# Kernel optimization log

Hardware: AMD Instinct MI355X
Metric: run time of the kernel (lower is better)

Reference implementation:

```python
import jax, jax.numpy as jnp
import numpy as np
from jax import lax

F8 = jnp.float8_e4m3fn


def setup_inputs() -> dict:
    key = jax.random.key(0)
    kx, kw = jax.random.split(key)
    x = jax.random.normal(kx, (2, 128, 4, 192, 320), dtype=jnp.float32)
    # matches reset_parameters: normal(0, 0.02) then cast to fp8
    weight = jax.random.normal(kw, (128, 128, 3, 3, 3), dtype=jnp.float32) * 0.02
    return {"x": x, "weight": weight}


def reference(x, weight):
    # fp8 e4m3 quantization round-trip (the torch module stores/consumes fp8),
    # compute/accumulate in fp32 as an fp8 conv kernel would.
    xq = x.astype(F8).astype(jnp.float32)
    wq = weight.astype(F8).astype(jnp.float32)
    # causal temporal padding: (kT-1, 0) = (2, 0); spatial 'same' padding (1,1)
    xp = jnp.pad(xq, ((0, 0), (0, 0), (2, 0), (1, 1), (1, 1)))
    out = lax.conv_general_dilated(
        xp, wq,
        window_strides=(1, 1, 1),
        padding='VALID',
        dimension_numbers=('NCDHW', 'OIDHW', 'NCDHW'),
    )  # (B, 128, 4, 192, 320)
    return out
```

## Files before the change

kernel.cpp:

```cpp
#include <hip/hip_runtime.h>
#include <hip/hip_fp8.h>


using f32x16 = __attribute__((ext_vector_type(16))) float;
using i32x8 = __attribute__((ext_vector_type(8))) int;
using i32x4 = __attribute__((ext_vector_type(4))) int;
typedef long long i64;
struct alignas(16) L2v { i64 x, y; };

namespace {
constexpr int Cc = 128, Dd = 4, Hh = 192, Ww = 320;
constexpr int HP = 194, WP = 322;
constexpr int NTAP = 27;
constexpr size_t PLANE = (size_t)4 * WP * 32;
constexpr size_t XQ_BYTES = (size_t)2 * Dd * HP * PLANE;
constexpr int ZA = 8 * 2 * 2576;
constexpr int ZB = 8 * 192 * 32;
constexpr int GSTR = WP * 32;
constexpr int HB = 1056;
constexpr int KDSTR = 9 * 2 * 4 * 64 * 32;
constexpr int NQX = 5 * 192 * 8;
constexpr int NZP = (ZA + ZB + 255) / 256;
constexpr int NWP = (Cc * Cc * NTAP + 255) / 256;
}

__global__ __launch_bounds__(256) void prep_kernel(const float* __restrict__ x,
                                                   const float* __restrict__ w,
                                                   unsigned char* __restrict__ xq,
                                                   unsigned char* __restrict__ wpk) {
  const int id = blockIdx.x;
  const int tid = threadIdx.x;
  if (id < NQX) {
    __shared__ unsigned char lt[64 * 136];
    const int wx = id % 5;
    const int h = (id / 5) % 192;
    const int bd = id / 960;
    const int b = bd >> 2, d = bd & 3;
    const int w0 = wx * 64;
    const int wl = tid & 63, cig = tid >> 6;
    const size_t cstr = (size_t)Dd * Hh * Ww;
    const float* xp = x + (((size_t)b * Cc * Dd + d) * Hh + h) * Ww + w0 + wl;
    #pragma unroll 4
    for (int i = 0; i < 32; ++i) {
      int ci = cig * 32 + i;
      __hip_fp8_e4m3 q(xp[ci * cstr]);
      lt[wl * 136 + ci] = q.__x;
    }
    __syncthreads();
    unsigned char* plane = xq + ((size_t)(b * Dd + d) * HP + h + 1) * PLANE;
    int g = tid >> 6, ww = tid & 63;
    const unsigned char* src = lt + ww * 136 + g * 32;
    i64 a0 = *(const i64*)(src), a1 = *(const i64*)(src + 8);
    i64 a2 = *(const i64*)(src + 16), a3 = *(const i64*)(src + 24);
    unsigned char* dst = plane + (size_t)g * GSTR + (size_t)(w0 + 1 + ww) * 32;
    *(L2v*)dst = L2v{a0, a1};
    *(L2v*)(dst + 16) = L2v{a2, a3};
  } else if (id < NQX + NZP) {
    int i = (id - NQX) * 256 + tid;
    if (i < ZA) {
      int bd = i / (2 * 2576);
      int r = i - bd * (2 * 2576);
      int hsel = r / 2576, seg = r - hsel * 2576;
      L2v z{0, 0};
      *(L2v*)(xq + ((size_t)bd * HP + (hsel ? 193 : 0)) * PLANE + (size_t)seg * 16) = z;
    } else if (i < ZA + ZB) {
      int j = i - ZA;
      int bd = j / (192 * 32);
      int r = j - bd * (192 * 32);
      int h = r / 32 + 1;
      int t = r & 31;
      int g = t >> 3, s2 = t & 7;
      int wsel = s2 >> 2, part = s2 & 3;
      *(i64*)(xq + ((size_t)bd * HP + h) * PLANE + (size_t)g * GSTR
              + (size_t)(wsel ? 321 : 0) * 32 + part * 8) = 0;
    }
  } else {
    int idx = (id - NQX - NZP) * 256 + tid;
    if (idx < Cc * Cc * NTAP) {
      int tap = idx % NTAP;
      int t = idx / NTAP;
      int ci = t % Cc, co = t / Cc;
      int cc = ci >> 6, cq = co >> 5;
      int lane = (((ci >> 5) & 1) << 5) | (co & 31);
      __hip_fp8_e4m3 q(w[idx]);
      wpk[((((size_t)tap * 2 + cc) * 4 + cq) * 64 + lane) * 32 + (ci & 31)] = q.__x;
    }
  }
}

__global__ __launch_bounds__(256, 2) void conv_mfma(const unsigned char* __restrict__ xq,
                                                    const unsigned char* __restrict__ wpk,
                                                    float* __restrict__ out) {
  __shared__ unsigned char lb[4 * 4 * 2 * HB];
  const int tid = threadIdx.x;
  const int lane = tid & 63, wv = tid >> 6;
  const int l31 = lane & 31, chalf = lane >> 5;
  const int hr = wv >> 1, ch = wv & 1;
  const int id = blockIdx.x;
  const int xcd = id & 7, j = id >> 3;
  const int h0l = j / 40, rem = j - h0l * 40;
  const int z = rem / 5, wx = rem - z * 5;
  const int b = z >> 2, dout = z & 3;
  const int h0 = (xcd * 12 + h0l) * 2;
  const int w0 = wx * 64;
  const int kdmin = dout >= 2 ? 0 : 2 - dout;

  const long imgstep = (long)HP * PLANE;
  const long img0 = (long)(b * Dd + dout - 2) * imgstep;
  const unsigned char* vbase = wpk + ch * 4096 + lane * 32;

  const unsigned char* bb[3];
  #pragma unroll
  for (int kw = 0; kw < 3; ++kw)
    bb[kw] = lb + (hr * 4 + chalf) * 2 * HB + (l31 + kw) * 16;

  f32x16 acc[2][2];
  #pragma unroll
  for (int a = 0; a < 2; ++a)
    #pragma unroll
    for (int n = 0; n < 2; ++n)
      #pragma unroll
      for (int r = 0; r < 16; ++r) acc[a][n][r] = 0.f;

  i32x8 av[3][2];

  for (int kd = kdmin; kd < 3; ++kd) {
    __syncthreads();
    const unsigned char* img = xq + img0 + (long)kd * imgstep;
    for (int u = tid; u < 1056; u += 256) {
      int w = u % 66, rest = u / 66;
      int g = rest & 3, hrow = rest >> 2;
      const unsigned char* src = img + (size_t)(h0 + hrow) * PLANE
          + (size_t)g * GSTR + (size_t)(w0 + w) * 32;
      L2v lo = *(const L2v*)src;
      L2v hi = *(const L2v*)(src + 16);
      unsigned char* base = lb + (hrow * 4 + g) * 2 * HB + w * 16;
      *(L2v*)(base) = lo;
      *(L2v*)(base + HB) = hi;
    }
    const unsigned char* wkd = vbase + (size_t)kd * KDSTR;
    #pragma unroll
    for (int t = 0; t < 2; ++t) {
      const int kh = t / 6, cc = (t / 3) % 2, kw = t % 3;
      #pragma unroll
      for (int ct = 0; ct < 2; ++ct)
        av[t][ct] = *(const i32x8*)(wkd + (kh * 3 + kw) * 16384 + cc * 8192 + ct * 2048);
    }
    asm volatile("s_waitcnt lgkmcnt(0)" ::: "memory");
    __builtin_amdgcn_s_barrier();
    __builtin_amdgcn_sched_barrier(0);

    __builtin_amdgcn_s_setprio(1);
    #pragma unroll
    for (int t = 0; t < 18; ++t) {
      const int kh = t / 6, cc = (t / 3) % 2, kw = t % 3;
      if (t < 16) {
        const int tp = t + 2;
        const int khp = tp / 6, ccp = (tp / 3) % 2, kwp = tp % 3;
        #pragma unroll
        for (int ct = 0; ct < 2; ++ct)
          av[tp % 3][ct] =
              *(const i32x8*)(wkd + (khp * 3 + kwp) * 16384 + ccp * 8192 + ct * 2048);
      }
      i32x8 bv[2];
      #pragma unroll
      for (int nf = 0; nf < 2; ++nf) {
        const int off = (kh * 4 + cc * 2) * 2 * HB + nf * 512;
        i32x4 blo = *(const i32x4*)(bb[kw] + off);
        i32x4 bhi = *(const i32x4*)(bb[kw] + off + HB);
        bv[nf] = __builtin_shufflevector(blo, bhi, 0, 1, 2, 3, 4, 5, 6, 7);
      }
      if (t < 16)      asm volatile("s_waitcnt vmcnt(4)" ::: "memory");
      else if (t == 16) asm volatile("s_waitcnt vmcnt(2)" ::: "memory");
      else              asm volatile("s_waitcnt vmcnt(0)" ::: "memory");
      asm volatile("s_waitcnt lgkmcnt(0)" ::: "memory");
      __builtin_amdgcn_sched_barrier(0);
      #pragma unroll
      for (int nf = 0; nf < 2; ++nf)
        #pragma unroll
        for (int ct = 0; ct < 2; ++ct)
          acc[ct][nf] = __builtin_amdgcn_mfma_scale_f32_32x32x64_f8f6f4(
              av[t % 3][ct], bv[nf], acc[ct][nf], 0, 0, 0, 127, 0, 127);
    }
    __builtin_amdgcn_s_setprio(0);
  }

  #pragma unroll
  for (int ct = 0; ct < 2; ++ct)
    #pragma unroll
    for (int nf = 0; nf < 2; ++nf) {
      int ww = w0 + nf * 32 + l31;
      #pragma unroll
      for (int reg = 0; reg < 16; ++reg) {
        int co = ch * 64 + ct * 32 + (reg & 3) + 8 * (reg >> 2) + 4 * chalf;
        out[(((size_t)b * Cc + co) * Dd + dout) * (size_t)(Hh * Ww)
            + (size_t)(h0 + hr) * Ww + ww] = acc[ct][nf][reg];
      }
    }
}

extern "C" void kernel_launch(void* const* d_in, const int* in_sizes, int n_in,
                              void* d_out, int out_size, void* d_ws, size_t ws_size,
                              hipStream_t stream) {
  const float* x = (const float*)d_in[0];
  const float* w = (const float*)d_in[1];
  unsigned char* xq = (unsigned char*)d_ws;
  unsigned char* wpk = xq + XQ_BYTES;
  float* out = (float*)d_out;

  prep_kernel<<<dim3(NQX + NZP + NWP), 256, 0, stream>>>(x, w, xq, wpk);
  conv_mfma<<<dim3(3840), 256, 0, stream>>>(xq, wpk, out);
}
```

Before: 222.9 us.

## Double-buffer LDS and weight fragments, drop manual waitcnts, raise occupancy to 3

```diff
diff --git a/kernel.cpp b/kernel.cpp
--- a/kernel.cpp
+++ b/kernel.cpp
@@ -88,7 +88,7 @@
   }
 }
 
-__global__ __launch_bounds__(256, 2) void conv_mfma(const unsigned char* __restrict__ xq,
+__global__ __launch_bounds__(256, 3) void conv_mfma(const unsigned char* __restrict__ xq,
                                                     const unsigned char* __restrict__ wpk,
                                                     float* __restrict__ out) {
   __shared__ unsigned char lb[4 * 4 * 2 * HB];
@@ -122,7 +122,28 @@
       #pragma unroll
       for (int r = 0; r < 16; ++r) acc[a][n][r] = 0.f;
 
-  i32x8 av[3][2];
+  i32x8 bvd[2][2];
+  i32x8 avd[2][2];
+
+#define LOADB(PAR, T)                                                          \
+  {                                                                            \
+    constexpr int kh_ = (T) / 6, cc_ = ((T) / 3) % 2, kw_ = (T) % 3;           \
+    _Pragma("unroll")                                                          \
+    for (int nf = 0; nf < 2; ++nf) {                                           \
+      const int off_ = (kh_ * 4 + cc_ * 2) * 2 * HB + nf * 512;                \
+      i32x4 blo_ = *(const i32x4*)(bb[kw_] + off_);                            \
+      i32x4 bhi_ = *(const i32x4*)(bb[kw_] + off_ + HB);                       \
+      bvd[PAR][nf] = __builtin_shufflevector(blo_, bhi_, 0, 1, 2, 3, 4, 5, 6, 7); \
+    }                                                                          \
+  }
+#define LOADA(PAR, T)                                                          \
+  {                                                                            \
+    constexpr int kh_ = (T) / 6, cc_ = ((T) / 3) % 2, kw_ = (T) % 3;           \
+    _Pragma("unroll")                                                          \
+    for (int ct = 0; ct < 2; ++ct)                                             \
+      avd[PAR][ct] = *(const i32x8*)(wkd + (kh_ * 3 + kw_) * 16384             \
+                                     + cc_ * 8192 + ct * 2048);                \
+  }
 
   for (int kd = kdmin; kd < 3; ++kd) {
     __syncthreads();
@@ -138,52 +159,46 @@
       *(L2v*)(base) = lo;
       *(L2v*)(base + HB) = hi;
     }
+    __syncthreads();
+
     const unsigned char* wkd = vbase + (size_t)kd * KDSTR;
-    #pragma unroll
-    for (int t = 0; t < 2; ++t) {
-      const int kh = t / 6, cc = (t / 3) % 2, kw = t % 3;
-      #pragma unroll
-      for (int ct = 0; ct < 2; ++ct)
-        av[t][ct] = *(const i32x8*)(wkd + (kh * 3 + kw) * 16384 + cc * 8192 + ct * 2048);
-    }
-    asm volatile("s_waitcnt lgkmcnt(0)" ::: "memory");
-    __builtin_amdgcn_s_barrier();
-    __builtin_amdgcn_sched_barrier(0);
-
+    LOADB(0, 0)
+    LOADA(0, 0)
     __builtin_amdgcn_s_setprio(1);
     #pragma unroll
     for (int t = 0; t < 18; ++t) {
-      const int kh = t / 6, cc = (t / 3) % 2, kw = t % 3;
-      if (t < 16) {
-        const int tp = t + 2;
-        const int khp = tp / 6, ccp = (tp / 3) % 2, kwp = tp % 3;
-        #pragma unroll
-        for (int ct = 0; ct < 2; ++ct)
-          av[tp % 3][ct] =
-              *(const i32x8*)(wkd + (khp * 3 + kwp) * 16384 + ccp * 8192 + ct * 2048);
+      const int p = t & 1, q = p ^ 1;
+      switch (t) {
+        case 0:  LOADB(1, 1)  LOADA(1, 1)  break;
+        case 1:  LOADB(0, 2)  LOADA(0, 2)  break;
+        case 2:  LOADB(1, 3)  LOADA(1, 3)  break;
+        case 3:  LOADB(0, 4)  LOADA(0, 4)  break;
+        case 4:  LOADB(1, 5)  LOADA(1, 5)  break;
+        case 5:  LOADB(0, 6)  LOADA(0, 6)  break;
+        case 6:  LOADB(1, 7)  LOADA(1, 7)  break;
+        case 7:  LOADB(0, 8)  LOADA(0, 8)  break;
+        case 8:  LOADB(1, 9)  LOADA(1, 9)  break;
+        case 9:  LOADB(0, 10) LOADA(0, 10) break;
+        case 10: LOADB(1, 11) LOADA(1, 11) break;
+        case 11: LOADB(0, 12) LOADA(0, 12) break;
+        case 12: LOADB(1, 13) LOADA(1, 13) break;
+        case 13: LOADB(0, 14) LOADA(0, 14) break;
+        case 14: LOADB(1, 15) LOADA(1, 15) break;
+        case 15: LOADB(0, 16) LOADA(0, 16) break;
+        case 16: LOADB(1, 17) LOADA(1, 17) break;
+        default: break;
       }
-      i32x8 bv[2];
-      #pragma unroll
-      for (int nf = 0; nf < 2; ++nf) {
-        const int off = (kh * 4 + cc * 2) * 2 * HB + nf * 512;
-        i32x4 blo = *(const i32x4*)(bb[kw] + off);
-        i32x4 bhi = *(const i32x4*)(bb[kw] + off + HB);
-        bv[nf] = __builtin_shufflevector(blo, bhi, 0, 1, 2, 3, 4, 5, 6, 7);
-      }
-      if (t < 16)      asm volatile("s_waitcnt vmcnt(4)" ::: "memory");
-      else if (t == 16) asm volatile("s_waitcnt vmcnt(2)" ::: "memory");
-      else              asm volatile("s_waitcnt vmcnt(0)" ::: "memory");
-      asm volatile("s_waitcnt lgkmcnt(0)" ::: "memory");
-      __builtin_amdgcn_sched_barrier(0);
       #pragma unroll
       for (int nf = 0; nf < 2; ++nf)
         #pragma unroll
         for (int ct = 0; ct < 2; ++ct)
           acc[ct][nf] = __builtin_amdgcn_mfma_scale_f32_32x32x64_f8f6f4(
-              av[t % 3][ct], bv[nf], acc[ct][nf], 0, 0, 0, 127, 0, 127);
+              avd[p][ct], bvd[p][nf], acc[ct][nf], 0, 0, 0, 127, 0, 127);
     }
     __builtin_amdgcn_s_setprio(0);
   }
+#undef LOADB
+#undef LOADA
 
   #pragma unroll
   for (int ct = 0; ct < 2; ++ct)
```

Result: no change. 225.7 us (+1.3%).

## Give each wave all 128 output channels over four output rows per block

Applied to the files above, without the earlier changes.

```diff
diff --git a/kernel.cpp b/kernel.cpp
--- a/kernel.cpp
+++ b/kernel.cpp
@@ -91,108 +91,91 @@
 __global__ __launch_bounds__(256, 2) void conv_mfma(const unsigned char* __restrict__ xq,
                                                     const unsigned char* __restrict__ wpk,
                                                     float* __restrict__ out) {
-  __shared__ unsigned char lb[4 * 4 * 2 * HB];
+  __shared__ unsigned char lb[6 * 4 * 2 * HB];
   const int tid = threadIdx.x;
-  const int lane = tid & 63, wv = tid >> 6;
+  const int lane = tid & 63;
+  const int hr = tid >> 6;
   const int l31 = lane & 31, chalf = lane >> 5;
-  const int hr = wv >> 1, ch = wv & 1;
   const int id = blockIdx.x;
   const int xcd = id & 7, j = id >> 3;
   const int h0l = j / 40, rem = j - h0l * 40;
   const int z = rem / 5, wx = rem - z * 5;
   const int b = z >> 2, dout = z & 3;
-  const int h0 = (xcd * 12 + h0l) * 2;
+  const int h0 = (xcd * 6 + h0l) * 4;
   const int w0 = wx * 64;
   const int kdmin = dout >= 2 ? 0 : 2 - dout;
 
   const long imgstep = (long)HP * PLANE;
   const long img0 = (long)(b * Dd + dout - 2) * imgstep;
-  const unsigned char* vbase = wpk + ch * 4096 + lane * 32;
+  const unsigned char* vbase = wpk + lane * 32;
 
   const unsigned char* bb[3];
   #pragma unroll
   for (int kw = 0; kw < 3; ++kw)
-    bb[kw] = lb + (hr * 4 + chalf) * 2 * HB + (l31 + kw) * 16;
+    bb[kw] = lb + hr * 8448 + chalf * 2112 + (l31 + kw) * 16;
 
-  f32x16 acc[2][2];
+  f32x16 acc[4][2];
   #pragma unroll
-  for (int a = 0; a < 2; ++a)
+  for (int a = 0; a < 4; ++a)
     #pragma unroll
     for (int n = 0; n < 2; ++n)
       #pragma unroll
       for (int r = 0; r < 16; ++r) acc[a][n][r] = 0.f;
 
-  i32x8 av[3][2];
-
   for (int kd = kdmin; kd < 3; ++kd) {
     __syncthreads();
     const unsigned char* img = xq + img0 + (long)kd * imgstep;
-    for (int u = tid; u < 1056; u += 256) {
+    for (int u = tid; u < 1584; u += 256) {
       int w = u % 66, rest = u / 66;
       int g = rest & 3, hrow = rest >> 2;
       const unsigned char* src = img + (size_t)(h0 + hrow) * PLANE
           + (size_t)g * GSTR + (size_t)(w0 + w) * 32;
       L2v lo = *(const L2v*)src;
       L2v hi = *(const L2v*)(src + 16);
-      unsigned char* base = lb + (hrow * 4 + g) * 2 * HB + w * 16;
+      unsigned char* base = lb + rest * 2112 + w * 16;
       *(L2v*)(base) = lo;
       *(L2v*)(base + HB) = hi;
     }
+    __syncthreads();
+
     const unsigned char* wkd = vbase + (size_t)kd * KDSTR;
-    #pragma unroll
-    for (int t = 0; t < 2; ++t) {
-      const int kh = t / 6, cc = (t / 3) % 2, kw = t % 3;
-      #pragma unroll
-      for (int ct = 0; ct < 2; ++ct)
-        av[t][ct] = *(const i32x8*)(wkd + (kh * 3 + kw) * 16384 + cc * 8192 + ct * 2048);
-    }
-    asm volatile("s_waitcnt lgkmcnt(0)" ::: "memory");
-    __builtin_amdgcn_s_barrier();
-    __builtin_amdgcn_sched_barrier(0);
-
     __builtin_amdgcn_s_setprio(1);
     #pragma unroll
-    for (int t = 0; t < 18; ++t) {
-      const int kh = t / 6, cc = (t / 3) % 2, kw = t % 3;
-      if (t < 16) {
-        const int tp = t + 2;
-        const int khp = tp / 6, ccp = (tp / 3) % 2, kwp = tp % 3;
+    for (int kh = 0; kh < 3; ++kh)
+      #pragma unroll
+      for (int cc = 0; cc < 2; ++cc)
         #pragma unroll
-        for (int ct = 0; ct < 2; ++ct)
-          av[tp % 3][ct] =
-              *(const i32x8*)(wkd + (khp * 3 + kwp) * 16384 + ccp * 8192 + ct * 2048);
-      }
-      i32x8 bv[2];
-      #pragma unroll
-      for (int nf = 0; nf < 2; ++nf) {
-        const int off = (kh * 4 + cc * 2) * 2 * HB + nf * 512;
-        i32x4 blo = *(const i32x4*)(bb[kw] + off);
-        i32x4 bhi = *(const i32x4*)(bb[kw] + off + HB);
-        bv[nf] = __builtin_shufflevector(blo, bhi, 0, 1, 2, 3, 4, 5, 6, 7);
-      }
-      if (t < 16)      asm volatile("s_waitcnt vmcnt(4)" ::: "memory");
-      else if (t == 16) asm volatile("s_waitcnt vmcnt(2)" ::: "memory");
-      else              asm volatile("s_waitcnt vmcnt(0)" ::: "memory");
-      asm volatile("s_waitcnt lgkmcnt(0)" ::: "memory");
-      __builtin_amdgcn_sched_barrier(0);
-      #pragma unroll
-      for (int nf = 0; nf < 2; ++nf)
-        #pragma unroll
-        for (int ct = 0; ct < 2; ++ct)
-          acc[ct][nf] = __builtin_amdgcn_mfma_scale_f32_32x32x64_f8f6f4(
-              av[t % 3][ct], bv[nf], acc[ct][nf], 0, 0, 0, 127, 0, 127);
-    }
+        for (int kw = 0; kw < 3; ++kw) {
+          i32x8 av[4];
+          #pragma unroll
+          for (int ct = 0; ct < 4; ++ct)
+            av[ct] = *(const i32x8*)(wkd + (kh * 3 + kw) * 16384 + cc * 8192 + ct * 2048);
+          i32x8 bv[2];
+          #pragma unroll
+          for (int nf = 0; nf < 2; ++nf) {
+            const int off = kh * 8448 + cc * 4224 + nf * 512;
+            i32x4 blo = *(const i32x4*)(bb[kw] + off);
+            i32x4 bhi = *(const i32x4*)(bb[kw] + off + HB);
+            bv[nf] = __builtin_shufflevector(blo, bhi, 0, 1, 2, 3, 4, 5, 6, 7);
+          }
+          #pragma unroll
+          for (int nf = 0; nf < 2; ++nf)
+            #pragma unroll
+            for (int ct = 0; ct < 4; ++ct)
+              acc[ct][nf] = __builtin_amdgcn_mfma_scale_f32_32x32x64_f8f6f4(
+                  av[ct], bv[nf], acc[ct][nf], 0, 0, 0, 127, 0, 127);
+        }
     __builtin_amdgcn_s_setprio(0);
   }
 
   #pragma unroll
-  for (int ct = 0; ct < 2; ++ct)
+  for (int ct = 0; ct < 4; ++ct)
     #pragma unroll
     for (int nf = 0; nf < 2; ++nf) {
       int ww = w0 + nf * 32 + l31;
       #pragma unroll
       for (int reg = 0; reg < 16; ++reg) {
-        int co = ch * 64 + ct * 32 + (reg & 3) + 8 * (reg >> 2) + 4 * chalf;
+        int co = ct * 32 + (reg & 3) + 8 * (reg >> 2) + 4 * chalf;
         out[(((size_t)b * Cc + co) * Dd + dout) * (size_t)(Hh * Ww)
             + (size_t)(h0 + hr) * Ww + ww] = acc[ct][nf][reg];
       }
@@ -209,5 +192,5 @@
   float* out = (float*)d_out;
 
   prep_kernel<<<dim3(NQX + NZP + NWP), 256, 0, stream>>>(x, w, xq, wpk);
-  conv_mfma<<<dim3(3840), 256, 0, stream>>>(xq, wpk, out);
+  conv_mfma<<<dim3(1920), 256, 0, stream>>>(xq, wpk, out);
 }
```

New measurement: 237.2 us. +6.4%, slower.
